# Kernel tuning notes

Hardware: AMD Instinct MI355X
Metric: run time of the kernel (lower is better)

Reference implementation:

```python
import jax, jax.numpy as jnp
import numpy as np

SCALES = (1, 2, 4, 8, 16, 32, 64, 128)
BETA = 0.25   # args.commit_beta
B, C, T = 64, 512, 128
Q, V = 8, 1024
DEPTH, K = 2, 3


def setup_inputs() -> dict:
    key = jax.random.key(0)
    k1, k2, k3, k4 = jax.random.split(key, 4)
    z = jax.random.normal(k1, (B, C, T), dtype=jnp.float32)
    codebooks = jax.random.normal(k2, (Q, V, C), dtype=jnp.float32)
    # small init so stacked ReLU convs stay numerically sane (fan_in = C*K)
    phi_w = jax.random.normal(k3, (Q, DEPTH, C, C, K), dtype=jnp.float32) * (1.0 / np.sqrt(C * K))
    phi_b = jax.random.normal(k4, (Q, DEPTH, C), dtype=jnp.float32) * 0.01
    return {"z": z, "codebooks": codebooks, "phi_w": phi_w, "phi_b": phi_b}


def _conv1d(x, w, b):
    # x: (B,C,T), w: (C_out,C_in,K), 'same' padding (K//2)
    y = jax.lax.conv_general_dilated(x, w, window_strides=(1,), padding=[(K // 2, K // 2)],
                                     dimension_numbers=('NCH', 'OIH', 'NCH'))
    return y + b[None, :, None]


def _phi(x, w_q, b_q):
    # Phi: DEPTH x (Conv1d + ReLU)
    for d in range(DEPTH):
        x = jax.nn.relu(_conv1d(x, w_q[d], b_q[d]))
    return x


def _quantize(xd, cb):
    # xd: (B,C,s) -> nearest codebook entry per timestep. cb: (V,C)
    s = xd.shape[-1]
    flat = xd.transpose(0, 2, 1).reshape(-1, C)                      # (B*s, C)
    d = (jnp.sum(flat * flat, axis=1, keepdims=True)
         - 2.0 * flat @ cb.T + jnp.sum(cb * cb, axis=1))            # (B*s, V)
    idx = jnp.argmin(d, axis=1)                                      # (B*s,)
    emb = cb[idx].reshape(B, s, C).transpose(0, 2, 1)                # (B,C,s)
    # straight-through (EMA codebook: no grad to codebook)
    quant = xd + jax.lax.stop_gradient(emb - xd)
    return quant, idx.reshape(B, s)


def reference(z, codebooks, phi_w, phi_b):
    z = z.astype(jnp.float32)
    z_ng = jax.lax.stop_gradient(z)
    z_q = z_ng
    z_hat = jnp.zeros_like(z_q)
    losses, usages, perps, all_idx = [], [], [], []
    for q, s in enumerate(SCALES):
        # area downsample == window mean (T divisible by s)
        xd = z_q.reshape(B, C, s, T // s).mean(axis=-1)              # (B,C,s)
        quant, idx = _quantize(xd, codebooks[q])
        up = quant if s == T else jax.image.resize(quant, (B, C, T), method='linear')
        z_hat_q = _phi(up, phi_w[q], phi_b[q])
        z_hat = z_hat + z_hat_q
        z_q = z_q - z_hat_q
        counts = jnp.zeros((V,), jnp.float32).at[idx.ravel()].add(1.0)
        usages.append(jnp.mean((counts > 0).astype(jnp.float32)) * 100.0)
        p = counts / (B * s)
        perps.append(jnp.exp(-jnp.sum(p * jnp.log(p + 1e-10))))
        losses.append(BETA * jnp.mean((jax.lax.stop_gradient(z_hat) - z) ** 2)
                      + jnp.mean((z_hat - z_ng) ** 2))
        all_idx.append(idx)
    nQ = float(len(SCALES))
    usage = sum(usages) / nQ
    loss = sum(losses) / nQ
    perp = sum(perps) / nQ
    z_hat_out = jax.lax.stop_gradient(z_hat) - z_ng + z              # straight-through output
    indices = jnp.concatenate([i for i in all_idx], axis=1)          # (B, sum(scales))
    return z_hat_out, usage, loss, perp, indices
```

## Files before the change

### kernel.cpp

```cpp
#include <hip/hip_runtime.h>
#include <math.h>

#define NB 64
#define NC 512
#define NT 128
#define NQ 8
#define NV 1024
#define NBIG 4194304
#define IDX_STRIDE 255

typedef _Float16 half_t;
typedef half_t f16x8 __attribute__((ext_vector_type(8)));
typedef float  f32x4 __attribute__((ext_vector_type(4)));

#define SC_MAIN 0.015625f
#define SC_MID  2.44140625e-4f

#define GLD16(g, l) __builtin_amdgcn_global_load_lds( \
    (const __attribute__((address_space(1))) unsigned int*)(g), \
    (__attribute__((address_space(3))) unsigned int*)(l), 16, 0, 0)

__device__ inline void split64(float v, half_t& h1, half_t& h2) {
    half_t a = (half_t)(v * 64.f);
    float r = v * 64.f - (float)a;
    h1 = a;
    h2 = (half_t)(r * 64.f);
}
__device__ inline void split1(float v, half_t& h1, half_t& h2) {
    half_t a = (half_t)v;
    float r = v - (float)a;
    h1 = a;
    h2 = (half_t)(r * 64.f);
}

__global__ void init_kernel(float* __restrict__ zhat, int* __restrict__ counts,
                            float* __restrict__ accums) {
    int i = blockIdx.x * 256 + threadIdx.x;
    const int stride = 2048 * 256;
    for (; i < NBIG; i += stride) {
        zhat[i] = 0.f;
        if (i < NQ * NV) counts[i] = 0;
        if (i < 16)      accums[i] = 0.f;
    }
}

__global__ void padzero_kernel(half_t* __restrict__ X1, half_t* __restrict__ X2) {
    int b = blockIdx.x;
    int row = blockIdx.y ? 129 : 0;
    int c = threadIdx.x;
    size_t off = ((size_t)b * 130 + row) * NC + c;
    X1[off] = (half_t)0.f; X2[off] = (half_t)0.f;
}

__global__ void cnorm_kernel(const float* __restrict__ cb, float* __restrict__ cnorm) {
    int wid  = (blockIdx.x * 256 + threadIdx.x) >> 6;
    int lane = threadIdx.x & 63;
    if (wid >= NQ * NV) return;
    const float* row = cb + (size_t)wid * NC;
    float s = 0.f;
    #pragma unroll
    for (int e = 0; e < NC / 64; ++e) { float v = row[lane + e * 64]; s = fmaf(v, v, s); }
    #pragma unroll
    for (int m = 32; m >= 1; m >>= 1) s += __shfl_xor(s, m, 64);
    if (lane == 0) cnorm[wid] = s;
}

__global__ void cbprep_kernel(const float* __restrict__ cb, half_t* __restrict__ CbT) {
    int idx = blockIdx.x * 256 + threadIdx.x;
    int e  = idx & 8191;
    int kt = (idx >> 13) & 7;
    int mt = (idx >> 16) & 7;
    int q  = idx >> 19;
    int m = e >> 6, kk = e & 63;
    int ci = kt * 64 + kk;
    int code = mt * 128 + m;
    float v = cb[((size_t)(q * NV + code)) * NC + ci];
    half_t h1, h2;
    split64(v, h1, h2);
    int off = ((m * 128 + kk * 2) ^ ((m & 7) << 4)) >> 1;
    size_t base = ((((size_t)q * 2 + 0) * 8 + mt) * 8 + kt) * 8192 + off;
    CbT[base] = h1;
    CbT[base + (size_t)8 * 8 * 8192] = h2;
}

__global__ __launch_bounds__(256) void downsample_split_kernel(
        const float* __restrict__ z, const float* __restrict__ zhat,
        half_t* __restrict__ Xd1, half_t* __restrict__ Xd2,
        int s, int log2s) {
    __shared__ float D[64 * 129];
    const int tid = threadIdx.x;
    const int b  = blockIdx.x;
    const int c0 = blockIdx.y << 6;
    const size_t gbase = ((size_t)(b * NC + c0)) * NT;
    #pragma unroll
    for (int i = 0; i < 8; ++i) {
        int idx4 = (i * 256 + tid) * 4;
        float4 zv = *(const float4*)(z    + gbase + idx4);
        float4 hv = *(const float4*)(zhat + gbase + idx4);
        int cc = idx4 >> 7, t = idx4 & 127;
        float* dp = D + cc * 129 + t;
        dp[0] = zv.x - hv.x; dp[1] = zv.y - hv.y; dp[2] = zv.z - hv.z; dp[3] = zv.w - hv.w;
    }
    __syncthreads();
    const int w = NT >> log2s;
    const float invw = 1.f / (float)w;
    for (int idx = tid; idx < (s << 6); idx += 256) {
        int cc = idx & 63;
        int j  = idx >> 6;
        const float* row = D + cc * 129 + j * w;
        float sum = 0.f;
        for (int i = 0; i < w; ++i) sum += row[i];
        float xd = sum * invw;
        half_t h1, h2;
        split1(xd, h1, h2);
        size_t o = ((size_t)(b * s + j)) * NC + c0 + cc;
        Xd1[o] = h1;
        Xd2[o] = h2;
    }
}

__global__ __launch_bounds__(256, 2) void quant_mfma_kernel(
        const half_t* __restrict__ CbTq,
        const half_t* __restrict__ Xd1, const half_t* __restrict__ Xd2,
        const float* __restrict__ cnorm,
        float* __restrict__ pval, int* __restrict__ pidx) {
    __shared__ half_t As1[8192];
    __shared__ half_t As2[8192];
    __shared__ half_t Bs1[4096];
    __shared__ half_t Bs2[4096];
    __shared__ float redv[2][2][2][16];
    __shared__ int   redi[2][2][2][16];
    const int tid = threadIdx.x;
    const int w = tid >> 6, l = tid & 63;
    const int wm = w >> 1, wn = w & 1;
    const int lane16 = l & 15, lhi = l >> 4;
    const int nblk = blockIdx.x, mt = blockIdx.y;
    const int r0 = nblk * 64;
    f32x4 accM[4][2] = {}, accm[4][2] = {};
    const half_t* C1b = CbTq + ((size_t)(0 * 8 + mt)) * (8 * 8192);
    const half_t* C2b = CbTq + ((size_t)(1 * 8 + mt)) * (8 * 8192);
    for (int kt = 0; kt < 8; ++kt) {
        const int ci0 = kt << 6;
        __syncthreads();
        const char* c1src = (const char*)(C1b + (size_t)kt * 8192);
        const char* c2src = (const char*)(C2b + (size_t)kt * 8192);
        #pragma unroll
        for (int i = 0; i < 4; ++i) {
            GLD16(c1src + (i * 256 + tid) * 16, (char*)As1 + i * 4096 + w * 1024);
            GLD16(c2src + (i * 256 + tid) * 16, (char*)As2 + i * 4096 + w * 1024);
        }
        #pragma unroll
        for (int i = 0; i < 2; ++i) {
            int c = i * 256 + tid;
            int n = c >> 3, sub = c & 7;
            size_t soff = ((size_t)(r0 + n)) * NC + ci0 + ((sub ^ (n & 7)) << 3);
            GLD16(Xd1 + soff, (char*)Bs1 + i * 4096 + w * 1024);
            GLD16(Xd2 + soff, (char*)Bs2 + i * 4096 + w * 1024);
        }
        __syncthreads();
        #pragma unroll
        for (int kstep = 0; kstep < 2; ++kstep) {
            const int kb = (kstep * 32 + lhi * 8) * 2;
            f16x8 a1[4], a2[4], b1[2], b2[2];
            #pragma unroll
            for (int im = 0; im < 4; ++im) {
                int m = wm * 64 + im * 16 + lane16;
                int off = (m * 128 + kb) ^ ((m & 7) << 4);
                a1[im] = *(const f16x8*)((const char*)As1 + off);
                a2[im] = *(const f16x8*)((const char*)As2 + off);
            }
            #pragma unroll
            for (int in = 0; in < 2; ++in) {
                int n = wn * 32 + in * 16 + lane16;
                int off = (n * 128 + kb) ^ ((n & 7) << 4);
                b1[in] = *(const f16x8*)((const char*)Bs1 + off);
                b2[in] = *(const f16x8*)((const char*)Bs2 + off);
            }
            #pragma unroll
            for (int im = 0; im < 4; ++im)
                #pragma unroll
                for (int in = 0; in < 2; ++in) {
                    accM[im][in] = __builtin_amdgcn_mfma_f32_16x16x32_f16(a1[im], b1[in], accM[im][in], 0, 0, 0);
                    accm[im][in] = __builtin_amdgcn_mfma_f32_16x16x32_f16(a1[im], b2[in], accm[im][in], 0, 0, 0);
                    accm[im][in] = __builtin_amdgcn_mfma_f32_16x16x32_f16(a2[im], b1[in], accm[im][in], 0, 0, 0);
                }
        }
    }
    float bv[2] = {1e30f, 1e30f};
    int   bi[2] = {0, 0};
    #pragma unroll
    for (int im = 0; im < 4; ++im) {
        int mb = mt * 128 + wm * 64 + im * 16 + lhi * 4;
        float4 cn = *(const float4*)(cnorm + mb);
        const float* cnp = (const float*)&cn;
        #pragma unroll
        for (int in = 0; in < 2; ++in) {
            #pragma unroll
            for (int r = 0; r < 4; ++r) {
                float d = cnp[r] - 2.f * (accM[im][in][r] * SC_MAIN + accm[im][in][r] * SC_MID);
                int code = mb + r;
                if (d < bv[in]) { bv[in] = d; bi[in] = code; }
            }
        }
    }
    #pragma unroll
    for (int m = 16; m <= 32; m <<= 1) {
        #pragma unroll
        for (int in = 0; in < 2; ++in) {
            float ov = __shfl_xor(bv[in], m, 64);
            int   oi = __shfl_xor(bi[in], m, 64);
            if (ov < bv[in] || (ov == bv[in] && oi < bi[in])) { bv[in] = ov; bi[in] = oi; }
        }
    }
    if (lhi == 0) {
        #pragma unroll
        for (int in = 0; in < 2; ++in) { redv[wm][wn][in][lane16] = bv[in]; redi[wm][wn][in][lane16] = bi[in]; }
    }
    __syncthreads();
    if (wm == 0 && lhi == 0) {
        #pragma unroll
        for (int in = 0; in < 2; ++in) {
            float v0 = redv[0][wn][in][lane16]; int i0 = redi[0][wn][in][lane16];
            float v1 = redv[1][wn][in][lane16]; int i1 = redi[1][wn][in][lane16];
            if (v1 < v0 || (v1 == v0 && i1 < i0)) { v0 = v1; i0 = i1; }
            int r = r0 + wn * 32 + in * 16 + lane16;
            pval[(size_t)r * 8 + mt] = v0;
            pidx[(size_t)r * 8 + mt] = i0;
        }
    }
}

__global__ void argmin_final_kernel(const float* __restrict__ pval, const int* __restrict__ pidx,
                                    int* __restrict__ idx_int, int* __restrict__ counts,
                                    float* __restrict__ out_idx, int R, int s, int log2s, int offq) {
    int r = blockIdx.x * 256 + threadIdx.x;
    if (r >= R) return;
    float bv = 1e30f; int bi = 0;
    #pragma unroll
    for (int k = 0; k < 8; ++k) {
        float v = pval[(size_t)r * 8 + k];
        int   i = pidx[(size_t)r * 8 + k];
        if (v < bv || (v == bv && i < bi)) { bv = v; bi = i; }
    }
    idx_int[r] = bi;
    atomicAdd(&counts[bi], 1);
    int b = r >> log2s, j = r & (s - 1);
    out_idx[(size_t)b * IDX_STRIDE + offq + j] = (float)bi;
}

__global__ void upsample_split_kernel(const float* __restrict__ cb, const int* __restrict__ idx_int,
                                      half_t* __restrict__ X1, half_t* __restrict__ X2, int s) {
    int b = blockIdx.x, tp = blockIdx.y, c = threadIdx.x;
    size_t off = ((size_t)b * 130 + tp) * NC + c;
    if (tp == 0 || tp == 129) { X1[off] = (half_t)0.f; X2[off] = (half_t)0.f; return; }
    int t = tp - 1;
    float in = (t + 0.5f) * ((float)s * (1.f / 128.f)) - 0.5f;
    float jf = floorf(in);
    float f = in - jf;
    int j0 = (int)jf;
    int i0 = min(max(j0, 0), s - 1);
    int i1 = min(max(j0 + 1, 0), s - 1);
    const int* ib = idx_int + b * s;
    float v0 = cb[(size_t)ib[i0] * NC + c];
    float v1 = cb[(size_t)ib[i1] * NC + c];
    float v = (1.f - f) * v0 + f * v1;
    half_t h1, h2;
    split1(v, h1, h2);
    X1[off] = h1; X2[off] = h2;
}

__global__ void wprep_kernel(const float* __restrict__ W ,
                             half_t* __restrict__ Wt) {
    int d = blockIdx.y;
    const float* Wd = W + (size_t)d * NC * NC * 3;
    half_t* Wtd = Wt + (size_t)d * (2 * 4 * 24 * 8192);
    int idx = blockIdx.x * 256 + threadIdx.x;
    int e  = idx & 8191;
    int rest = idx >> 13;
    int kt = rest % 24;
    int mtl = rest / 24;
    int m = e >> 6, kk = e & 63;
    int k = kt * 64 + kk;
    int ks = k >> 9, ci = k & 511;
    int co = mtl * 128 + m;
    float v = Wd[((size_t)co * NC + ci) * 3 + ks];
    half_t h1, h2;
    split64(v, h1, h2);
    int off = ((m * 128 + kk * 2) ^ ((m & 7) << 4)) >> 1;
    size_t base = ((size_t)mtl * 24 + kt) * 8192 + off;
    Wtd[base] = h1;
    Wtd[base + (size_t)4 * 24 * 8192] = h2;
}

template<int MODE>
__global__ __launch_bounds__(256, 2) void conv_mfma_kernel(
        const half_t* __restrict__ Wt,
        const half_t* __restrict__ X1, const half_t* __restrict__ X2,
        const float* __restrict__ bias,
        half_t* __restrict__ Y1, half_t* __restrict__ Y2,
        float* __restrict__ zhat, const float* __restrict__ z,
        float* __restrict__ lpart) {
    __shared__ half_t As1[8192];
    __shared__ half_t As2[8192];
    __shared__ half_t Bs1[4096];
    __shared__ half_t Bs2[4096];
    const int tid = threadIdx.x;
    const int w = tid >> 6, l = tid & 63;
    const int wm = w >> 1, wn = w & 1;
    const int lane16 = l & 15, lhi = l >> 4;
    const int nblk = blockIdx.x, mt = blockIdx.y;
    const int b = nblk >> 1, t0 = (nblk & 1) << 6;
    f32x4 accM[4][2] = {}, accm[4][2] = {};
    const half_t* W1b = Wt + ((size_t)(0 * 4 + mt)) * (24 * 8192);
    const half_t* W2b = Wt + ((size_t)(1 * 4 + mt)) * (24 * 8192);
    for (int kt = 0; kt < 24; ++kt) {
        const int ks  = kt >> 3;
        const int ci0 = (kt & 7) << 6;
        const int rowb = b * 130 + t0 + ks;
        __syncthreads();
        const char* w1src = (const char*)(W1b + (size_t)kt * 8192);
        const char* w2src = (const char*)(W2b + (size_t)kt * 8192);
        #pragma unroll
        for (int i = 0; i < 4; ++i) {
            GLD16(w1src + (i * 256 + tid) * 16, (char*)As1 + i * 4096 + w * 1024);
            GLD16(w2src + (i * 256 + tid) * 16, (char*)As2 + i * 4096 + w * 1024);
        }
        #pragma unroll
        for (int i = 0; i < 2; ++i) {
            int c = i * 256 + tid;
            int n = c >> 3, sub = c & 7;
            size_t soff = ((size_t)(rowb + n)) * NC + ci0 + ((sub ^ (n & 7)) << 3);
            GLD16(X1 + soff, (char*)Bs1 + i * 4096 + w * 1024);
            GLD16(X2 + soff, (char*)Bs2 + i * 4096 + w * 1024);
        }
        __syncthreads();
        #pragma unroll
        for (int kstep = 0; kstep < 2; ++kstep) {
            const int kb = (kstep * 32 + lhi * 8) * 2;
            f16x8 a1[4], a2[4], b1[2], b2[2];
            #pragma unroll
            for (int im = 0; im < 4; ++im) {
                int m = wm * 64 + im * 16 + lane16;
                int off = (m * 128 + kb) ^ ((m & 7) << 4);
                a1[im] = *(const f16x8*)((const char*)As1 + off);
                a2[im] = *(const f16x8*)((const char*)As2 + off);
            }
            #pragma unroll
            for (int in = 0; in < 2; ++in) {
                int n = wn * 32 + in * 16 + lane16;
                int off = (n * 128 + kb) ^ ((n & 7) << 4);
                b1[in] = *(const f16x8*)((const char*)Bs1 + off);
                b2[in] = *(const f16x8*)((const char*)Bs2 + off);
            }
            #pragma unroll
            for (int im = 0; im < 4; ++im)
                #pragma unroll
                for (int in = 0; in < 2; ++in) {
                    accM[im][in] = __builtin_amdgcn_mfma_f32_16x16x32_f16(a1[im], b1[in], accM[im][in], 0, 0, 0);
                    accm[im][in] = __builtin_amdgcn_mfma_f32_16x16x32_f16(a1[im], b2[in], accm[im][in], 0, 0, 0);
                    accm[im][in] = __builtin_amdgcn_mfma_f32_16x16x32_f16(a2[im], b1[in], accm[im][in], 0, 0, 0);
                }
        }
    }
    float lsum = 0.f;
    #pragma unroll
    for (int im = 0; im < 4; ++im) {
        int mb = mt * 128 + wm * 64 + im * 16 + lhi * 4;
        float bs[4];
        #pragma unroll
        for (int r = 0; r < 4; ++r) bs[r] = bias[mb + r];
        #pragma unroll
        for (int in = 0; in < 2; ++in) {
            int t = t0 + wn * 32 + in * 16 + lane16;
            if (MODE == 0) {
                half_t h1v[4], h2v[4];
                #pragma unroll
                for (int r = 0; r < 4; ++r) {
                    float y = accM[im][in][r] * SC_MAIN + accm[im][in][r] * SC_MID + bs[r];
                    y = y > 0.f ? y : 0.f;
                    split1(y, h1v[r], h2v[r]);
                }
                size_t rowoff = ((size_t)(b * 130 + 1 + t)) * NC + mb;
                *(ushort4*)(Y1 + rowoff) = *(const ushort4*)h1v;
                *(ushort4*)(Y2 + rowoff) = *(const ushort4*)h2v;
            } else {
                size_t base = ((size_t)b * NC + mb) * NT + t;
                #pragma unroll
                for (int r = 0; r < 4; ++r) {
                    float y = accM[im][in][r] * SC_MAIN + accm[im][in][r] * SC_MID + bs[r];
                    y = y > 0.f ? y : 0.f;
                    size_t oi = base + (size_t)r * NT;
                    float zn = zhat[oi] + y;
                    zhat[oi] = zn;
                    float d = zn - z[oi];
                    lsum = fmaf(d, d, lsum);
                }
            }
        }
    }
    if (MODE == 1) {
        __syncthreads();
        float* red = (float*)As1;
        red[tid] = lsum;
        __syncthreads();
        for (int st = 128; st >= 1; st >>= 1) {
            if (tid < st) red[tid] += red[tid + st];
            __syncthreads();
        }
        if (tid == 0) lpart[blockIdx.y * 128 + blockIdx.x] = red[0];
    }
}

__global__ void scale_final_kernel(const float* __restrict__ lpart, const int* __restrict__ counts,
                                   float* __restrict__ accums, float invBS) {
    __shared__ float sm[256];
    __shared__ float se[256];
    __shared__ int   su[256];
    int tid = threadIdx.x;
    float ls = lpart[tid] + lpart[tid + 256];
    int used = 0; float ent = 0.f;
    #pragma unroll
    for (int k = 0; k < 4; ++k) {
        int cv = counts[tid + k * 256];
        if (cv > 0) used++;
        float p = (float)cv * invBS;
        ent = fmaf(p, logf(p + 1e-10f), ent);
    }
    sm[tid] = ls; se[tid] = ent; su[tid] = used;
    __syncthreads();
    for (int st = 128; st >= 1; st >>= 1) {
        if (tid < st) { sm[tid] += sm[tid + st]; se[tid] += se[tid + st]; su[tid] += su[tid + st]; }
        __syncthreads();
    }
    if (tid == 0) {
        float m = sm[0] * (1.f / (float)NBIG);
        accums[1] += 0.25f * m + m;
        accums[0] += ((float)su[0] * (1.f / 1024.f)) * 100.f;
        accums[2] += expf(-se[0]);
    }
}

__global__ void final_write_kernel(const float* __restrict__ accums, float* __restrict__ outscal) {
    int t = threadIdx.x;
    if (t < 3) outscal[t] = accums[t] * 0.125f;
}

extern "C" void kernel_launch(void* const* d_in, const int* in_sizes, int n_in,
                              void* d_out, int out_size, void* d_ws, size_t ws_size,
                              hipStream_t stream) {
    const float* z  = (const float*)d_in[0];
    const float* cb = (const float*)d_in[1];
    const float* pw = (const float*)d_in[2];
    const float* pb = (const float*)d_in[3];

    float* zhat     = (float*)d_out;
    float* out_scal = zhat + NBIG;
    float* out_idx  = zhat + NBIG + 3;

    char* w = (char*)d_ws;
    half_t* Xd1 = (half_t*)w;  w += (size_t)8192 * NC * 2;
    half_t* Xd2 = (half_t*)w;  w += (size_t)8192 * NC * 2;
    half_t* Xa1 = (half_t*)w;  w += (size_t)NB * 130 * NC * 2;
    half_t* Xa2 = (half_t*)w;  w += (size_t)NB * 130 * NC * 2;
    half_t* Xb1 = (half_t*)w;  w += (size_t)NB * 130 * NC * 2;
    half_t* Xb2 = (half_t*)w;  w += (size_t)NB * 130 * NC * 2;
    half_t* Wt  = (half_t*)w;  w += (size_t)2 * 2 * 4 * 24 * 8192 * 2;
    half_t* CbT = (half_t*)w;  w += (size_t)NQ * 2 * 8 * 8 * 8192 * 2;
    float* pval  = (float*)w;  w += (size_t)8192 * 8 * 4;
    int*   pidx  = (int*)w;    w += (size_t)8192 * 8 * 4;
    int*   idx_i = (int*)w;    w += (size_t)16384 * 4;
    int*   counts= (int*)w;    w += (size_t)NQ * NV * 4;
    float* cnorm = (float*)w;  w += (size_t)NQ * NV * 4;
    float* lpart = (float*)w;  w += (size_t)512 * 4;
    float* accums= (float*)w;  w += 256;

    init_kernel<<<2048, 256, 0, stream>>>(zhat, counts, accums);
    padzero_kernel<<<dim3(64, 2), 512, 0, stream>>>(Xb1, Xb2);
    cnorm_kernel<<<(NQ * NV) / 4, 256, 0, stream>>>(cb, cnorm);
    cbprep_kernel<<<16384, 256, 0, stream>>>(cb, CbT);

    const size_t WT_CONV = (size_t)2 * 4 * 24 * 8192;
    int offq = 0;
    for (int q = 0; q < NQ; ++q) {
        int s = 1 << q;
        int R = NB * s;
        const float* cbq = cb + (size_t)q * NV * NC;
        const float* wq  = pw + (size_t)q * 2 * NC * NC * 3;
        const float* bq0 = pb + (size_t)q * 2 * NC;
        const float* bq1 = bq0 + NC;

        downsample_split_kernel<<<dim3(64, 8), 256, 0, stream>>>(z, zhat, Xd1, Xd2, s, q);
        quant_mfma_kernel<<<dim3(R / 64, 8), 256, 0, stream>>>(
            CbT + (size_t)q * 2 * 8 * 8 * 8192, Xd1, Xd2, cnorm + q * NV, pval, pidx);
        argmin_final_kernel<<<(R + 255) / 256, 256, 0, stream>>>(pval, pidx, idx_i,
                                                                 counts + q * NV, out_idx, R, s, q, offq);
        upsample_split_kernel<<<dim3(64, 130), 512, 0, stream>>>(cbq, idx_i, Xa1, Xa2, s);
        wprep_kernel<<<dim3(3072, 2), 256, 0, stream>>>(wq, Wt);
        conv_mfma_kernel<0><<<dim3(128, 4), 256, 0, stream>>>(
            Wt, Xa1, Xa2, bq0, Xb1, Xb2, nullptr, nullptr, nullptr);
        conv_mfma_kernel<1><<<dim3(128, 4), 256, 0, stream>>>(
            Wt + WT_CONV, Xb1, Xb2, bq1, nullptr, nullptr, zhat, z, lpart);
        scale_final_kernel<<<1, 256, 0, stream>>>(lpart, counts + q * NV, accums, 1.f / (float)(NB * s));
        offq += s;
    }
    final_write_kernel<<<1, 64, 0, stream>>>(accums, out_scal);
}
```

Measured before the change: 1.050 ms.

## Double-buffer conv MFMA tiles and enlarge blocks to 512 threads covering full T

The conv kernel now uses 512-thread blocks that each cover a full batch row (128 timesteps), so each weight tile is loaded once per 128 columns instead of once per 64. LDS is double-buffered: the next K-tile is prefetched with global_load_lds while the current one is computed, leaving one barrier per tile instead of two. The grid is halved and the loss partial reduction is resized to match. LDS use grows to 128 KB per block, so occupancy drops to one block per CU, and the grid of 256 blocks may underfill the GPU.

```diff
diff --git a/kernel.cpp b/kernel.cpp
--- a/kernel.cpp
+++ b/kernel.cpp
@@ -293,64 +293,58 @@
 }
 
 template<int MODE>
-__global__ __launch_bounds__(256, 2) void conv_mfma_kernel(
+__global__ __launch_bounds__(512, 2) void conv_mfma_kernel(
         const half_t* __restrict__ Wt,
         const half_t* __restrict__ X1, const half_t* __restrict__ X2,
         const float* __restrict__ bias,
         half_t* __restrict__ Y1, half_t* __restrict__ Y2,
         float* __restrict__ zhat, const float* __restrict__ z,
         float* __restrict__ lpart) {
-    __shared__ half_t As1[8192];
-    __shared__ half_t As2[8192];
-    __shared__ half_t Bs1[4096];
-    __shared__ half_t Bs2[4096];
+    __shared__ half_t A1a[8192], A2a[8192], B1a[8192], B2a[8192];
+    __shared__ half_t A1b[8192], A2b[8192], B1b[8192], B2b[8192];
     const int tid = threadIdx.x;
-    const int w = tid >> 6, l = tid & 63;
-    const int wm = w >> 1, wn = w & 1;
-    const int lane16 = l & 15, lhi = l >> 4;
-    const int nblk = blockIdx.x, mt = blockIdx.y;
-    const int b = nblk >> 1, t0 = (nblk & 1) << 6;
+    const int w = tid >> 6;
+    const int wm = w >> 2, wn = w & 3;
+    const int l = tid & 63, lane16 = l & 15, lhi = l >> 4;
+    const int b = blockIdx.x, mt = blockIdx.y;
     f32x4 accM[4][2] = {}, accm[4][2] = {};
     const half_t* W1b = Wt + ((size_t)(0 * 4 + mt)) * (24 * 8192);
     const half_t* W2b = Wt + ((size_t)(1 * 4 + mt)) * (24 * 8192);
-    for (int kt = 0; kt < 24; ++kt) {
-        const int ks  = kt >> 3;
-        const int ci0 = (kt & 7) << 6;
-        const int rowb = b * 130 + t0 + ks;
-        __syncthreads();
-        const char* w1src = (const char*)(W1b + (size_t)kt * 8192);
-        const char* w2src = (const char*)(W2b + (size_t)kt * 8192);
-        #pragma unroll
-        for (int i = 0; i < 4; ++i) {
-            GLD16(w1src + (i * 256 + tid) * 16, (char*)As1 + i * 4096 + w * 1024);
-            GLD16(w2src + (i * 256 + tid) * 16, (char*)As2 + i * 4096 + w * 1024);
-        }
+
+    auto stage = [&](half_t* dA1, half_t* dA2, half_t* dB1, half_t* dB2, int kt) {
+        const int ks = kt >> 3, ci0 = (kt & 7) << 6;
+        const char* s1 = (const char*)(W1b + (size_t)kt * 8192);
+        const char* s2 = (const char*)(W2b + (size_t)kt * 8192);
+        const int rowb0 = b * 130 + ks;
         #pragma unroll
         for (int i = 0; i < 2; ++i) {
-            int c = i * 256 + tid;
-            int n = c >> 3, sub = c & 7;
-            size_t soff = ((size_t)(rowb + n)) * NC + ci0 + ((sub ^ (n & 7)) << 3);
-            GLD16(X1 + soff, (char*)Bs1 + i * 4096 + w * 1024);
-            GLD16(X2 + soff, (char*)Bs2 + i * 4096 + w * 1024);
-        }
-        __syncthreads();
+            int doff = i * 8192 + w * 1024;
+            GLD16(s1 + (i * 512 + tid) * 16, (char*)dA1 + doff);
+            GLD16(s2 + (i * 512 + tid) * 16, (char*)dA2 + doff);
+            int c = i * 512 + tid, n = c >> 3, sub = c & 7;
+            size_t soff = (size_t)(rowb0 + n) * NC + ci0 + ((sub ^ (n & 7)) << 3);
+            GLD16(X1 + soff, (char*)dB1 + doff);
+            GLD16(X2 + soff, (char*)dB2 + doff);
+        }
+    };
+    auto compute = [&](const half_t* A1, const half_t* A2, const half_t* B1, const half_t* B2) {
         #pragma unroll
         for (int kstep = 0; kstep < 2; ++kstep) {
-            const int kb = (kstep * 32 + lhi * 8) * 2;
+            const int kb = kstep * 64 + lhi * 16;
             f16x8 a1[4], a2[4], b1[2], b2[2];
             #pragma unroll
             for (int im = 0; im < 4; ++im) {
                 int m = wm * 64 + im * 16 + lane16;
                 int off = (m * 128 + kb) ^ ((m & 7) << 4);
-                a1[im] = *(const f16x8*)((const char*)As1 + off);
-                a2[im] = *(const f16x8*)((const char*)As2 + off);
+                a1[im] = *(const f16x8*)((const char*)A1 + off);
+                a2[im] = *(const f16x8*)((const char*)A2 + off);
             }
             #pragma unroll
             for (int in = 0; in < 2; ++in) {
                 int n = wn * 32 + in * 16 + lane16;
                 int off = (n * 128 + kb) ^ ((n & 7) << 4);
-                b1[in] = *(const f16x8*)((const char*)Bs1 + off);
-                b2[in] = *(const f16x8*)((const char*)Bs2 + off);
+                b1[in] = *(const f16x8*)((const char*)B1 + off);
+                b2[in] = *(const f16x8*)((const char*)B2 + off);
             }
             #pragma unroll
             for (int im = 0; im < 4; ++im)
@@ -361,7 +355,20 @@
                     accm[im][in] = __builtin_amdgcn_mfma_f32_16x16x32_f16(a2[im], b1[in], accm[im][in], 0, 0, 0);
                 }
         }
-    }
+    };
+
+    stage(A1a, A2a, B1a, B2a, 0);
+    __syncthreads();
+    #pragma unroll 1
+    for (int k2 = 0; k2 < 12; ++k2) {
+        stage(A1b, A2b, B1b, B2b, 2 * k2 + 1);
+        compute(A1a, A2a, B1a, B2a);
+        __syncthreads();
+        if (k2 < 11) stage(A1a, A2a, B1a, B2a, 2 * k2 + 2);
+        compute(A1b, A2b, B1b, B2b);
+        __syncthreads();
+    }
+
     float lsum = 0.f;
     #pragma unroll
     for (int im = 0; im < 4; ++im) {
@@ -371,7 +378,7 @@
         for (int r = 0; r < 4; ++r) bs[r] = bias[mb + r];
         #pragma unroll
         for (int in = 0; in < 2; ++in) {
-            int t = t0 + wn * 32 + in * 16 + lane16;
+            int t = wn * 32 + in * 16 + lane16;
             if (MODE == 0) {
                 half_t h1v[4], h2v[4];
                 #pragma unroll
@@ -400,14 +407,14 @@
     }
     if (MODE == 1) {
         __syncthreads();
-        float* red = (float*)As1;
+        float* red = (float*)A1a;
         red[tid] = lsum;
         __syncthreads();
-        for (int st = 128; st >= 1; st >>= 1) {
+        for (int st = 256; st >= 1; st >>= 1) {
             if (tid < st) red[tid] += red[tid + st];
             __syncthreads();
         }
-        if (tid == 0) lpart[blockIdx.y * 128 + blockIdx.x] = red[0];
+        if (tid == 0) lpart[blockIdx.y * 64 + blockIdx.x] = red[0];
     }
 }
 
@@ -417,7 +424,7 @@
     __shared__ float se[256];
     __shared__ int   su[256];
     int tid = threadIdx.x;
-    float ls = lpart[tid] + lpart[tid + 256];
+    float ls = lpart[tid];
     int used = 0; float ent = 0.f;
     #pragma unroll
     for (int k = 0; k < 4; ++k) {
@@ -471,7 +478,7 @@
     int*   idx_i = (int*)w;    w += (size_t)16384 * 4;
     int*   counts= (int*)w;    w += (size_t)NQ * NV * 4;
     float* cnorm = (float*)w;  w += (size_t)NQ * NV * 4;
-    float* lpart = (float*)w;  w += (size_t)512 * 4;
+    float* lpart = (float*)w;  w += (size_t)256 * 4;
     float* accums= (float*)w;  w += 256;
 
     init_kernel<<<2048, 256, 0, stream>>>(zhat, counts, accums);
@@ -496,9 +503,9 @@
                                                                  counts + q * NV, out_idx, R, s, q, offq);
         upsample_split_kernel<<<dim3(64, 130), 512, 0, stream>>>(cbq, idx_i, Xa1, Xa2, s);
         wprep_kernel<<<dim3(3072, 2), 256, 0, stream>>>(wq, Wt);
-        conv_mfma_kernel<0><<<dim3(128, 4), 256, 0, stream>>>(
+        conv_mfma_kernel<0><<<dim3(64, 4), 512, 0, stream>>>(
             Wt, Xa1, Xa2, bq0, Xb1, Xb2, nullptr, nullptr, nullptr);
-        conv_mfma_kernel<1><<<dim3(128, 4), 256, 0, stream>>>(
+        conv_mfma_kernel<1><<<dim3(64, 4), 512, 0, stream>>>(
             Wt + WT_CONV, Xb1, Xb2, bq1, nullptr, nullptr, zhat, z, lpart);
         scale_final_kernel<<<1, 256, 0, stream>>>(lpart, counts + q * NV, accums, 1.f / (float)(NB * s));
         offq += s;
```

After: 1.022 ms. 1.03x faster.
